# Optimization experiments

Measured on AMD Instinct MI355X. Metric: run time of the kernel, lower is better.

## Reference

```python
import jax, jax.numpy as jnp
import numpy as np

B, S, D, H = 2, 2048, 1024, 16
HD = D // H  # head_dim = 64


def setup_inputs() -> dict:
    key = jax.random.key(0)
    ks = jax.random.split(key, 10)
    std = 1.0 / np.sqrt(D)
    inputs = jax.random.normal(ks[0], (B, S, D), dtype=jnp.float32)
    # stacked per-head projection weights: [H, HD, D] (row-major like nn.Linear)
    Wq = jax.random.uniform(ks[1], (H, HD, D), jnp.float32, -std, std)
    bq = jax.random.uniform(ks[2], (H, HD), jnp.float32, -std, std)
    Wk = jax.random.uniform(ks[3], (H, HD, D), jnp.float32, -std, std)
    bk = jax.random.uniform(ks[4], (H, HD), jnp.float32, -std, std)
    Wv = jax.random.uniform(ks[5], (H, HD, D), jnp.float32, -std, std)
    bv = jax.random.uniform(ks[6], (H, HD), jnp.float32, -std, std)
    Wo = jax.random.uniform(ks[7], (D, D), jnp.float32, -std, std)
    bo = jax.random.uniform(ks[8], (D,), jnp.float32, -std, std)
    return {"inputs": inputs, "Wq": Wq, "bq": bq, "Wk": Wk, "bk": bk,
            "Wv": Wv, "bv": bv, "Wo": Wo, "bo": bo}


def reference(inputs, Wq, bq, Wk, bk, Wv, bv, Wo, bo):
    # per-head projections, batched over heads: [B,H,S,HD]
    q = jnp.einsum('bsd,hed->bhse', inputs, Wq) + bq[None, :, None, :]
    k = jnp.einsum('bsd,hed->bhse', inputs, Wk) + bk[None, :, None, :]
    v = jnp.einsum('bsd,hed->bhse', inputs, Wv) + bv[None, :, None, :]
    scale = 1.0 / np.sqrt(HD).astype(np.float32)
    # explicit [B,H,S,S] score matrix, as in the original naive attention
    scores = jnp.einsum('bhqe,bhke->bhqk', q, k) * scale
    causal = jnp.tril(jnp.ones((S, S), dtype=bool))
    scores = jnp.where(causal[None, None], scores, jnp.float32(-jnp.inf))
    attn = jax.nn.softmax(scores, axis=-1)  # dropout p=0 -> identity
    wv = jnp.einsum('bhqk,bhke->bhqe', attn, v)
    # concat heads along feature dim: [B,S,H*HD] = [B,S,D]
    z = wv.transpose(0, 2, 1, 3).reshape(B, S, D)
    out = jnp.einsum('bsd,ed->bse', z, Wo) + bo
    return out
```

## Files before the change

kernel.cpp:

```cpp
#include <hip/hip_runtime.h>
#include <math.h>

#define Bx 2
#define Sx 2048
#define Dx 1024
#define Hx 16
#define HDx 64
#define Mx (Bx*Sx)

typedef __bf16 bf16x8 __attribute__((ext_vector_type(8)));
typedef __bf16 bf16x4 __attribute__((ext_vector_type(4)));
typedef float  f32x4  __attribute__((ext_vector_type(4)));

#define SCL 0.18033688011112042f

__device__ __forceinline__ void gload_lds16(const __bf16* g, __bf16* l) {
  __builtin_amdgcn_global_load_lds(
      (const __attribute__((address_space(1))) unsigned int*)g,
      (__attribute__((address_space(3))) unsigned int*)l, 16, 0, 0);
}

__device__ __forceinline__ void cvt8(const float* s, __bf16* d) {
  float4 a = *(const float4*)s;
  float4 b = *(const float4*)(s + 4);
  bf16x8 o;
  o[0] = (__bf16)a.x; o[1] = (__bf16)a.y; o[2] = (__bf16)a.z; o[3] = (__bf16)a.w;
  o[4] = (__bf16)b.x; o[5] = (__bf16)b.y; o[6] = (__bf16)b.z; o[7] = (__bf16)b.w;
  *(bf16x8*)d = o;
}

__global__ __launch_bounds__(256) void cvt_kernel(
    const float* __restrict__ x, const float* __restrict__ Wq,
    const float* __restrict__ Wk, const float* __restrict__ Wv,
    const float* __restrict__ Wo, const float* __restrict__ bq,
    const float* __restrict__ bk, const float* __restrict__ bv,
    __bf16* __restrict__ xb, __bf16* __restrict__ wqkv,
    __bf16* __restrict__ wob, float* __restrict__ bqkv)
{
  const int bid = blockIdx.x;
  const int t = threadIdx.x;
  const size_t MEG = 1024u * 1024u;
  if (bid < 2048) {
    size_t e = (size_t)bid * 2048 + t * 8;
    cvt8(x + e, xb + e);
  } else if (bid < 3584) {
    size_t e = (size_t)(bid - 2048) * 2048 + t * 8;
    const float* src = (e < MEG) ? (Wq + e) : (e < 2 * MEG) ? (Wk + (e - MEG)) : (Wv + (e - 2 * MEG));
    cvt8(src, wqkv + e);
  } else if (bid < 4096) {
    size_t e = (size_t)(bid - 3584) * 2048 + t * 8;
    cvt8(Wo + e, wob + e);
  } else {
    for (int i = t; i < 3072; i += 256)
      bqkv[i] = (i < 1024) ? bq[i] : (i < 2048) ? bk[i - 1024] : bv[i - 2048];
  }
}

template<int TM, int TN, int MODE>
__global__ __launch_bounds__(256) void gemm_k(
    const __bf16* __restrict__ A, const __bf16* __restrict__ W,
    const float* __restrict__ bias, float* __restrict__ Cf,
    __bf16* __restrict__ Cb, __bf16* __restrict__ vT,
    int M, int N, int K, int ldc)
{
  __shared__ __align__(16) char smem[2 * (TM + TN) * 64 * 2];
  __bf16* AsB = (__bf16*)smem;

  constexpr int MS = TM / 32;
  constexpr int NS = TN / 32;
  const int tid = threadIdx.x;
  const int lane = tid & 63, wave = tid >> 6;
  const int l16 = lane & 15, quad = lane >> 4;
  const int wm = (wave >> 1) * (TM / 2);
  const int wn = (wave & 1) * (TN / 2);
  const int swz = l16 & 7;

  const int lid = blockIdx.y * gridDim.x + blockIdx.x;
  const int g8 = lid >> 6;
  const int r64 = lid & 63;
  const int gpm = (int)gridDim.y >> 3;
  const int gm = g8 % gpm;
  const int gn = g8 / gpm;
  const int m0 = (gm * 8 + (r64 & 7)) * TM;
  const int n0 = (gn * 8 + (r64 >> 3)) * TN;

  const f32x4 zero = {0.f, 0.f, 0.f, 0.f};
  f32x4 acc[MS][NS];
#pragma unroll
  for (int i = 0; i < MS; ++i)
#pragma unroll
    for (int j = 0; j < NS; ++j) acc[i][j] = zero;

  const int srow = tid >> 3;
  const int scs = (tid & 7) ^ (srow & 7);
  const __bf16* Ag = A + (size_t)(m0 + srow) * K + scs * 8;
  const __bf16* Wg = W + (size_t)(n0 + srow) * K + scs * 8;

#define G_STAGE(k0_, b_)                                                        \
  { __bf16* As_ = AsB + (b_) * (TM + TN) * 64;                                  \
    __bf16* Bs_ = As_ + TM * 64;                                                \
    _Pragma("unroll")                                                           \
    for (int i = 0; i < TM / 32; ++i)                                           \
      gload_lds16(Ag + (size_t)(i * 32) * K + (k0_), &As_[(i * 256 + tid) * 8]);\
    _Pragma("unroll")                                                           \
    for (int i = 0; i < TN / 32; ++i)                                           \
      gload_lds16(Wg + (size_t)(i * 32) * K + (k0_), &Bs_[(i * 256 + tid) * 8]); }

  const int NT = K >> 6;
  G_STAGE(0, 0)
  __syncthreads();

  for (int t = 0; t < NT; ++t) {
    if (t + 1 < NT) G_STAGE((t + 1) << 6, (t + 1) & 1)
    const __bf16* As_ = AsB + (t & 1) * (TM + TN) * 64;
    const __bf16* Bs_ = As_ + TM * 64;
#pragma unroll
    for (int hk = 0; hk < 2; ++hk) {
      const int ph = ((hk * 4 + quad) ^ swz) * 8;
      bf16x8 af[MS], bfr[NS];
#pragma unroll
      for (int i = 0; i < MS; ++i)
        af[i] = *(const bf16x8*)&As_[(wm + i * 16 + l16) * 64 + ph];
#pragma unroll
      for (int j = 0; j < NS; ++j)
        bfr[j] = *(const bf16x8*)&Bs_[(wn + j * 16 + l16) * 64 + ph];
#pragma unroll
      for (int i = 0; i < MS; ++i)
#pragma unroll
        for (int j = 0; j < NS; ++j)
          acc[i][j] = __builtin_amdgcn_mfma_f32_16x16x32_bf16(af[i], bfr[j], acc[i][j], 0, 0, 0);
    }
    __syncthreads();
  }

  if (MODE == 0) {
    float* Cs = (float*)smem;
    constexpr int cst = TN + 4;
#pragma unroll
    for (int j = 0; j < NS; ++j) {
      const int c = wn + j * 16 + l16;
      const float bv_ = bias[n0 + c];
#pragma unroll
      for (int i = 0; i < MS; ++i) {
        const int r0 = wm + i * 16 + quad * 4;
#pragma unroll
        for (int g = 0; g < 4; ++g)
          Cs[(r0 + g) * cst + c] = acc[i][j][g] + bv_;
      }
    }
    __syncthreads();
    constexpr int passes = TM * TN / (256 * 4);
#pragma unroll
    for (int p = 0; p < passes; ++p) {
      const int slot = p * 256 + tid;
      const int row = slot / (TN / 4);
      const int col4 = (slot % (TN / 4)) * 4;
      f32x4 v = *(const f32x4*)&Cs[row * cst + col4];
      *(f32x4*)&Cf[(size_t)(m0 + row) * ldc + n0 + col4] = v;
    }
  } else {
    __bf16* Cs = (__bf16*)smem;
    constexpr int cst = TN + 8;
    const bool vtile = (n0 >= 2048);
    if (!vtile) {
#pragma unroll
      for (int j = 0; j < NS; ++j) {
        const int c = wn + j * 16 + l16;
        const float bv_ = bias[n0 + c];
        const float sc = ((n0 + c) < 1024) ? SCL : 1.0f;
#pragma unroll
        for (int i = 0; i < MS; ++i) {
          const int r0 = wm + i * 16 + quad * 4;
#pragma unroll
          for (int g = 0; g < 4; ++g)
            Cs[(r0 + g) * cst + c] = (__bf16)((acc[i][j][g] + bv_) * sc);
        }
      }
      __syncthreads();
      constexpr int passes = TM * TN / (256 * 8);
#pragma unroll
      for (int p = 0; p < passes; ++p) {
        const int slot = p * 256 + tid;
        const int row = slot / (TN / 8);
        const int col8 = (slot % (TN / 8)) * 8;
        bf16x8 v = *(const bf16x8*)&Cs[row * cst + col8];
        *(bf16x8*)&Cb[(size_t)(m0 + row) * 3072 + n0 + col8] = v;
      }
    } else {
      constexpr int cstT = TM + 8;
#pragma unroll
      for (int j = 0; j < NS; ++j) {
        const int c = wn + j * 16 + l16;
        const float bv_ = bias[n0 + c];
#pragma unroll
        for (int i = 0; i < MS; ++i) {
          const int r0 = wm + i * 16 + quad * 4;
#pragma unroll
          for (int g = 0; g < 4; ++g)
            Cs[c * cstT + r0 + g] = (__bf16)(acc[i][j][g] + bv_);
        }
      }
      __syncthreads();
      const int bb = m0 >> 11, ml = m0 & 2047;
      constexpr int passes = TM * TN / (256 * 8);
#pragma unroll
      for (int p = 0; p < passes; ++p) {
        const int slot = p * 256 + tid;
        const int dd = slot / (TM / 8);
        const int ss8 = (slot % (TM / 8)) * 8;
        bf16x8 v = *(const bf16x8*)&Cs[dd * cstT + ss8];
        const int c2 = n0 - 2048 + dd;
        const int hh = c2 >> 6, ddd = c2 & 63;
        *(bf16x8*)&vT[((size_t)(bb * 16 + hh) * 64 + ddd) * 2048 + ml + ss8] = v;
      }
    }
  }
}

__global__ __launch_bounds__(256) void attn_mfma(
    const __bf16* __restrict__ qkv, const __bf16* __restrict__ vT,
    __bf16* __restrict__ zb)
{
  __shared__ __bf16 Qs[64 * 64];
  __shared__ __bf16 Ks[2][64 * 64];
  __shared__ __bf16 Vs[3][64 * 64];

  const int tid = threadIdx.x;
  const int lane = tid & 63, wave = tid >> 6;
  const int l16 = lane & 15, quad = lane >> 4;
  const int bx = blockIdx.x;
  const int qt = 31 - (bx >> 5);
  const int bh = bx & 31;
  const int h = bh & 15, b = bh >> 4;
  const int q0 = qt * 64;

  const __bf16* qg = qkv + (size_t)b * 2048 * 3072 + h * 64;
  const __bf16* kg = qg + 1024;
  const __bf16* vg = vT + (size_t)bh * 64 * 2048;

#define STAGE_KV(kt_, kbuf, vbuf)                                               \
  { const int kn = (kt_) * 64;                                                  \
    _Pragma("unroll")                                                           \
    for (int i = 0; i < 2; ++i) {                                               \
      int slot = i * 256 + tid;                                                 \
      int row = slot >> 3, ph2 = slot & 7;                                      \
      int cs = ph2 ^ (row & 7);                                                 \
      gload_lds16(kg + (size_t)(kn + row) * 3072 + cs * 8, &Ks[kbuf][slot * 8]);\
      gload_lds16(vg + (size_t)row * 2048 + kn + cs * 8, &Vs[vbuf][slot * 8]);  \
    } }

#pragma unroll
  for (int i = 0; i < 2; ++i) {
    int slot = i * 256 + tid;
    int row = slot >> 3, ph2 = slot & 7;
    int cs = ph2 ^ (row & 7);
    gload_lds16(qg + (size_t)(q0 + row) * 3072 + cs * 8, &Qs[slot * 8]);
  }
  STAGE_KV(0, 0, 0)
  __syncthreads();

  const int swz = l16 & 7;
  const int sw0 = ((quad) ^ swz) * 8;
  const int sw1 = ((quad + 4) ^ swz) * 8;
  const int mrow = wave * 16 + l16;

  bf16x8 qf0 = *(const bf16x8*)&Qs[mrow * 64 + sw0];
  bf16x8 qf1 = *(const bf16x8*)&Qs[mrow * 64 + sw1];
  __bf16* P = &Qs[wave * 16 * 64];

  bf16x8 onesf;
  {
    __bf16 ov = (l16 == 0) ? (__bf16)1.0f : (__bf16)0.0f;
#pragma unroll
    for (int i = 0; i < 8; ++i) onesf[i] = ov;
  }

  const f32x4 zero = {0.f, 0.f, 0.f, 0.f};
  f32x4 O[4], Ol = zero;
#pragma unroll
  for (int j = 0; j < 4; ++j) O[j] = zero;
  f32x4 s_cur[4], s_next[4];

#define S_TILE(sdst, kb)                                                        \
  { _Pragma("unroll")                                                           \
    for (int m = 0; m < 4; ++m) sdst[m] = zero;                                 \
    _Pragma("unroll")                                                           \
    for (int m = 0; m < 4; ++m) {                                               \
      bf16x8 kf0 = *(const bf16x8*)&Ks[kb][(m * 16 + l16) * 64 + sw0];          \
      sdst[m] = __builtin_amdgcn_mfma_f32_16x16x32_bf16(kf0, qf0, sdst[m],0,0,0);\
      bf16x8 kf1 = *(const bf16x8*)&Ks[kb][(m * 16 + l16) * 64 + sw1];          \
      sdst[m] = __builtin_amdgcn_mfma_f32_16x16x32_bf16(kf1, qf1, sdst[m],0,0,0);\
    } }

#define EXP_P(s, DIAG)                                                          \
  { _Pragma("unroll")                                                           \
    for (int m = 0; m < 4; ++m) {                                               \
      const int kl = m * 16 + quad * 4;                                         \
      bf16x4 st;                                                                \
      _Pragma("unroll")                                                         \
      for (int g = 0; g < 4; ++g) {                                             \
        float p = __builtin_exp2f(s[m][g]);                                     \
        if (DIAG && (kl + g) > (wave * 16 + l16)) p = 0.f;                      \
        st[g] = (__bf16)p;                                                      \
      }                                                                         \
      *(bf16x4*)&P[l16 * 64 + (((2 * m + (quad >> 1)) ^ swz) * 8) + (quad & 1) * 4] = st; \
    } }

#define PV_TILE(vb)                                                             \
  { bf16x8 pf0 = *(const bf16x8*)&P[l16 * 64 + sw0];                            \
    bf16x8 pf1 = *(const bf16x8*)&P[l16 * 64 + sw1];                            \
    _Pragma("unroll")                                                           \
    for (int j = 0; j < 4; ++j) {                                               \
      bf16x8 vf0 = *(const bf16x8*)&Vs[vb][(j * 16 + l16) * 64 + sw0];          \
      O[j] = __builtin_amdgcn_mfma_f32_16x16x32_bf16(pf0, vf0, O[j], 0, 0, 0);  \
      bf16x8 vf1 = *(const bf16x8*)&Vs[vb][(j * 16 + l16) * 64 + sw1];          \
      O[j] = __builtin_amdgcn_mfma_f32_16x16x32_bf16(pf1, vf1, O[j], 0, 0, 0);  \
    }                                                                           \
    Ol = __builtin_amdgcn_mfma_f32_16x16x32_bf16(pf0, onesf, Ol, 0, 0, 0);      \
    Ol = __builtin_amdgcn_mfma_f32_16x16x32_bf16(pf1, onesf, Ol, 0, 0, 0); }

  if (qt > 0) STAGE_KV(1, 1, 1)
  S_TILE(s_cur, 0)
  if (qt > 0) __syncthreads();

  for (int t = 0; t < qt; ++t) {
    EXP_P(s_cur, false)
    S_TILE(s_next, (t + 1) & 1)
    PV_TILE(t % 3)
    if (t + 2 <= qt) STAGE_KV(t + 2, t & 1, (t + 2) % 3)
    __syncthreads();
#pragma unroll
    for (int m = 0; m < 4; ++m) s_cur[m] = s_next[m];
  }
  EXP_P(s_cur, true)
  PV_TILE(qt % 3)

  const int rq = q0 + wave * 16 + quad * 4;
#pragma unroll
  for (int g = 0; g < 4; ++g) {
    const float lv = __shfl(Ol[g], quad * 16);
    const float inv = 1.0f / lv;
    const size_t rb = (size_t)(b * 2048 + rq + g) * 1024 + h * 64 + l16;
#pragma unroll
    for (int j = 0; j < 4; ++j)
      zb[rb + j * 16] = (__bf16)(O[j][g] * inv);
  }
}

extern "C" void kernel_launch(void* const* d_in, const int* in_sizes, int n_in,
                              void* d_out, int out_size, void* d_ws, size_t ws_size,
                              hipStream_t stream) {
  (void)in_sizes; (void)n_in; (void)out_size; (void)ws_size;
  const float* x  = (const float*)d_in[0];
  const float* Wq = (const float*)d_in[1];
  const float* bq = (const float*)d_in[2];
  const float* Wk = (const float*)d_in[3];
  const float* bk = (const float*)d_in[4];
  const float* Wv = (const float*)d_in[5];
  const float* bv = (const float*)d_in[6];
  const float* Wo = (const float*)d_in[7];
  const float* bo = (const float*)d_in[8];

  char* ws = (char*)d_ws;
  __bf16* xb   = (__bf16*)(ws);
  __bf16* wqkv = (__bf16*)(ws + (8ull  << 20));
  __bf16* wob  = (__bf16*)(ws + (14ull << 20));
  float*  bqkv = (float*) (ws + (16ull << 20));
  __bf16* qkv  = (__bf16*)(ws + (17ull << 20));
  __bf16* vT   = (__bf16*)(ws + (41ull << 20));
  __bf16* zb   = (__bf16*)(ws + (49ull << 20));

  cvt_kernel<<<4097, 256, 0, stream>>>(x, Wq, Wk, Wv, Wo, bq, bk, bv,
                                       xb, wqkv, wob, bqkv);
  gemm_k<128, 128, 1><<<dim3(24, 32), 256, 0, stream>>>(
      xb, wqkv, bqkv, nullptr, qkv, vT, Mx, 3072, 1024, 0);
  attn_mfma<<<1024, 256, 0, stream>>>(qkv, vT, zb);
  gemm_k<128, 64, 0><<<dim3(16, 32), 256, 0, stream>>>(
      zb, wob, bo, (float*)d_out, nullptr, nullptr, Mx, 1024, 1024, 1024);
}
```

Baseline: 177.2 us.

## Widen attention query tile to 128 rows per block to reuse K/V tiles

After: 188.1 us. 1.06x slower.

```diff
diff --git a/kernel.cpp b/kernel.cpp
--- a/kernel.cpp
+++ b/kernel.cpp
@@ -217,11 +217,11 @@
   }
 }
 
-__global__ __launch_bounds__(256) void attn_mfma(
+__global__ __launch_bounds__(256, 2) void attn_mfma(
     const __bf16* __restrict__ qkv, const __bf16* __restrict__ vT,
     __bf16* __restrict__ zb)
 {
-  __shared__ __bf16 Qs[64 * 64];
+  __shared__ __bf16 Qs[128 * 64];
   __shared__ __bf16 Ks[2][64 * 64];
   __shared__ __bf16 Vs[3][64 * 64];
 
@@ -229,10 +229,12 @@
   const int lane = tid & 63, wave = tid >> 6;
   const int l16 = lane & 15, quad = lane >> 4;
   const int bx = blockIdx.x;
-  const int qt = 31 - (bx >> 5);
-  const int bh = bx & 31;
+  const int jj = bx & 255;
+  const int bh = jj & 31;
+  const int gg = jj >> 5;
+  const int qt = (bx >> 8) ? gg : (15 - gg);
+  const int q0 = qt * 128;
   const int h = bh & 15, b = bh >> 4;
-  const int q0 = qt * 64;
 
   const __bf16* qg = qkv + (size_t)b * 2048 * 3072 + h * 64;
   const __bf16* kg = qg + 1024;
@@ -250,7 +252,7 @@
     } }
 
 #pragma unroll
-  for (int i = 0; i < 2; ++i) {
+  for (int i = 0; i < 4; ++i) {
     int slot = i * 256 + tid;
     int row = slot >> 3, ph2 = slot & 7;
     int cs = ph2 ^ (row & 7);
@@ -260,13 +262,17 @@
   __syncthreads();
 
   const int swz = l16 & 7;
-  const int sw0 = ((quad) ^ swz) * 8;
+  const int sw0 = (quad ^ swz) * 8;
   const int sw1 = ((quad + 4) ^ swz) * 8;
-  const int mrow = wave * 16 + l16;
-
-  bf16x8 qf0 = *(const bf16x8*)&Qs[mrow * 64 + sw0];
-  bf16x8 qf1 = *(const bf16x8*)&Qs[mrow * 64 + sw1];
-  __bf16* P = &Qs[wave * 16 * 64];
+
+  bf16x8 qf0[2], qf1[2];
+#pragma unroll
+  for (int n = 0; n < 2; ++n) {
+    const int r = wave * 32 + n * 16 + l16;
+    qf0[n] = *(const bf16x8*)&Qs[r * 64 + sw0];
+    qf1[n] = *(const bf16x8*)&Qs[r * 64 + sw1];
+  }
+  __bf16* P = &Qs[wave * 32 * 64];
 
   bf16x8 onesf;
   {
@@ -276,74 +282,97 @@
   }
 
   const f32x4 zero = {0.f, 0.f, 0.f, 0.f};
-  f32x4 O[4], Ol = zero;
-#pragma unroll
-  for (int j = 0; j < 4; ++j) O[j] = zero;
-  f32x4 s_cur[4], s_next[4];
+  f32x4 O[4][2], Ol[2];
+#pragma unroll
+  for (int j = 0; j < 4; ++j) { O[j][0] = zero; O[j][1] = zero; }
+  Ol[0] = zero; Ol[1] = zero;
+  f32x4 s_cur[4][2], s_next[4][2];
 
 #define S_TILE(sdst, kb)                                                        \
   { _Pragma("unroll")                                                           \
-    for (int m = 0; m < 4; ++m) sdst[m] = zero;                                 \
-    _Pragma("unroll")                                                           \
     for (int m = 0; m < 4; ++m) {                                               \
       bf16x8 kf0 = *(const bf16x8*)&Ks[kb][(m * 16 + l16) * 64 + sw0];          \
-      sdst[m] = __builtin_amdgcn_mfma_f32_16x16x32_bf16(kf0, qf0, sdst[m],0,0,0);\
       bf16x8 kf1 = *(const bf16x8*)&Ks[kb][(m * 16 + l16) * 64 + sw1];          \
-      sdst[m] = __builtin_amdgcn_mfma_f32_16x16x32_bf16(kf1, qf1, sdst[m],0,0,0);\
-    } }
-
-#define EXP_P(s, DIAG)                                                          \
+      _Pragma("unroll")                                                         \
+      for (int n = 0; n < 2; ++n) {                                             \
+        sdst[m][n] = zero;                                                      \
+        sdst[m][n] = __builtin_amdgcn_mfma_f32_16x16x32_bf16(kf0, qf0[n], sdst[m][n],0,0,0); \
+        sdst[m][n] = __builtin_amdgcn_mfma_f32_16x16x32_bf16(kf1, qf1[n], sdst[m][n],0,0,0); \
+      } } }
+
+#define EXP_P(s, DIAG, KOFF)                                                    \
   { _Pragma("unroll")                                                           \
     for (int m = 0; m < 4; ++m) {                                               \
-      const int kl = m * 16 + quad * 4;                                         \
-      bf16x4 st;                                                                \
+      const int kl = (KOFF) + m * 16 + quad * 4;                                \
       _Pragma("unroll")                                                         \
-      for (int g = 0; g < 4; ++g) {                                             \
-        float p = __builtin_exp2f(s[m][g]);                                     \
-        if (DIAG && (kl + g) > (wave * 16 + l16)) p = 0.f;                      \
-        st[g] = (__bf16)p;                                                      \
-      }                                                                         \
-      *(bf16x4*)&P[l16 * 64 + (((2 * m + (quad >> 1)) ^ swz) * 8) + (quad & 1) * 4] = st; \
-    } }
+      for (int n = 0; n < 2; ++n) {                                             \
+        const int ql = wave * 32 + n * 16 + l16;                                \
+        bf16x4 st;                                                              \
+        _Pragma("unroll")                                                       \
+        for (int g = 0; g < 4; ++g) {                                           \
+          float p = __builtin_exp2f(s[m][n][g]);                                \
+          if (DIAG && (kl + g) > ql) p = 0.f;                                   \
+          st[g] = (__bf16)p;                                                    \
+        }                                                                       \
+        *(bf16x4*)&P[n * 1024 + l16 * 64 + (((2 * m + (quad >> 1)) ^ swz) * 8) + (quad & 1) * 4] = st; \
+      } } }
 
 #define PV_TILE(vb)                                                             \
-  { bf16x8 pf0 = *(const bf16x8*)&P[l16 * 64 + sw0];                            \
-    bf16x8 pf1 = *(const bf16x8*)&P[l16 * 64 + sw1];                            \
+  { bf16x8 pf0[2], pf1[2];                                                      \
+    _Pragma("unroll")                                                           \
+    for (int n = 0; n < 2; ++n) {                                               \
+      pf0[n] = *(const bf16x8*)&P[n * 1024 + l16 * 64 + sw0];                   \
+      pf1[n] = *(const bf16x8*)&P[n * 1024 + l16 * 64 + sw1];                   \
+    }                                                                           \
     _Pragma("unroll")                                                           \
     for (int j = 0; j < 4; ++j) {                                               \
       bf16x8 vf0 = *(const bf16x8*)&Vs[vb][(j * 16 + l16) * 64 + sw0];          \
-      O[j] = __builtin_amdgcn_mfma_f32_16x16x32_bf16(pf0, vf0, O[j], 0, 0, 0);  \
       bf16x8 vf1 = *(const bf16x8*)&Vs[vb][(j * 16 + l16) * 64 + sw1];          \
-      O[j] = __builtin_amdgcn_mfma_f32_16x16x32_bf16(pf1, vf1, O[j], 0, 0, 0);  \
+      _Pragma("unroll")                                                         \
+      for (int n = 0; n < 2; ++n) {                                             \
+        O[j][n] = __builtin_amdgcn_mfma_f32_16x16x32_bf16(pf0[n], vf0, O[j][n], 0, 0, 0); \
+        O[j][n] = __builtin_amdgcn_mfma_f32_16x16x32_bf16(pf1[n], vf1, O[j][n], 0, 0, 0); \
+      }                                                                         \
     }                                                                           \
-    Ol = __builtin_amdgcn_mfma_f32_16x16x32_bf16(pf0, onesf, Ol, 0, 0, 0);      \
-    Ol = __builtin_amdgcn_mfma_f32_16x16x32_bf16(pf1, onesf, Ol, 0, 0, 0); }
-
-  if (qt > 0) STAGE_KV(1, 1, 1)
+    _Pragma("unroll")                                                           \
+    for (int n = 0; n < 2; ++n) {                                               \
+      Ol[n] = __builtin_amdgcn_mfma_f32_16x16x32_bf16(pf0[n], onesf, Ol[n], 0, 0, 0); \
+      Ol[n] = __builtin_amdgcn_mfma_f32_16x16x32_bf16(pf1[n], onesf, Ol[n], 0, 0, 0); \
+    } }
+
+  const int NT = 2 * qt + 2;
+
+  STAGE_KV(1, 1, 1)
   S_TILE(s_cur, 0)
-  if (qt > 0) __syncthreads();
-
-  for (int t = 0; t < qt; ++t) {
-    EXP_P(s_cur, false)
-    S_TILE(s_next, (t + 1) & 1)
+  __syncthreads();
+
+  for (int t = 0; t < NT - 1; ++t) {
+    if (t < NT - 2) { EXP_P(s_cur, false, 0) }
+    else            { EXP_P(s_cur, true, 0) }
+    if (t < NT - 2 || wave >= 2) S_TILE(s_next, (t + 1) & 1)
     PV_TILE(t % 3)
-    if (t + 2 <= qt) STAGE_KV(t + 2, t & 1, (t + 2) % 3)
+    if (t + 2 < NT) STAGE_KV(t + 2, t & 1, (t + 2) % 3)
     __syncthreads();
 #pragma unroll
-    for (int m = 0; m < 4; ++m) s_cur[m] = s_next[m];
-  }
-  EXP_P(s_cur, true)
-  PV_TILE(qt % 3)
-
-  const int rq = q0 + wave * 16 + quad * 4;
-#pragma unroll
-  for (int g = 0; g < 4; ++g) {
-    const float lv = __shfl(Ol[g], quad * 16);
-    const float inv = 1.0f / lv;
-    const size_t rb = (size_t)(b * 2048 + rq + g) * 1024 + h * 64 + l16;
-#pragma unroll
-    for (int j = 0; j < 4; ++j)
-      zb[rb + j * 16] = (__bf16)(O[j][g] * inv);
+    for (int m = 0; m < 4; ++m) { s_cur[m][0] = s_next[m][0]; s_cur[m][1] = s_next[m][1]; }
+  }
+  if (wave >= 2) {
+    EXP_P(s_cur, true, 64)
+    PV_TILE((NT - 1) % 3)
+  }
+
+#pragma unroll
+  for (int n = 0; n < 2; ++n) {
+    const int rq = q0 + wave * 32 + n * 16 + quad * 4;
+#pragma unroll
+    for (int g = 0; g < 4; ++g) {
+      const float lv = __shfl(Ol[n][g], quad * 16);
+      const float inv = 1.0f / lv;
+      const size_t rb = (size_t)(b * 2048 + rq + g) * 1024 + h * 64 + l16;
+#pragma unroll
+      for (int j = 0; j < 4; ++j)
+        zb[rb + j * 16] = (__bf16)(O[j][n][g] * inv);
+    }
   }
 }
 
@@ -374,7 +403,7 @@
                                        xb, wqkv, wob, bqkv);
   gemm_k<128, 128, 1><<<dim3(24, 32), 256, 0, stream>>>(
       xb, wqkv, bqkv, nullptr, qkv, vT, Mx, 3072, 1024, 0);
-  attn_mfma<<<1024, 256, 0, stream>>>(qkv, vT, zb);
+  attn_mfma<<<512, 256, 0, stream>>>(qkv, vT, zb);
   gemm_k<128, 64, 0><<<dim3(16, 32), 256, 0, stream>>>(
       zb, wob, bo, (float*)d_out, nullptr, nullptr, Mx, 1024, 1024, 1024);
 }
```

## Rebalance attention tile order, double-buffer V, and raise MFMA priority

Applied to the files above, without the earlier changes.

Result: slower. 183.2 us (+3.4%).

```diff
diff --git a/kernel.cpp b/kernel.cpp
--- a/kernel.cpp
+++ b/kernel.cpp
@@ -217,20 +217,22 @@
   }
 }
 
-__global__ __launch_bounds__(256) void attn_mfma(
+__global__ __launch_bounds__(256, 4) void attn_mfma(
     const __bf16* __restrict__ qkv, const __bf16* __restrict__ vT,
     __bf16* __restrict__ zb)
 {
   __shared__ __bf16 Qs[64 * 64];
   __shared__ __bf16 Ks[2][64 * 64];
-  __shared__ __bf16 Vs[3][64 * 64];
+  __shared__ __bf16 Vs[2][64 * 64];
 
   const int tid = threadIdx.x;
   const int lane = tid & 63, wave = tid >> 6;
   const int l16 = lane & 15, quad = lane >> 4;
   const int bx = blockIdx.x;
-  const int qt = 31 - (bx >> 5);
   const int bh = bx & 31;
+  const int s8 = (bx >> 5) & 7;
+  const int p4 = bx >> 8;
+  const int qt = (p4 == 0) ? s8 : (p4 == 1) ? 15 - s8 : (p4 == 2) ? 16 + s8 : 31 - s8;
   const int h = bh & 15, b = bh >> 4;
   const int q0 = qt * 64;
 
@@ -238,7 +240,7 @@
   const __bf16* kg = qg + 1024;
   const __bf16* vg = vT + (size_t)bh * 64 * 2048;
 
-#define STAGE_KV(kt_, kbuf, vbuf)                                               \
+#define STAGE_K(kt_, kbuf)                                                      \
   { const int kn = (kt_) * 64;                                                  \
     _Pragma("unroll")                                                           \
     for (int i = 0; i < 2; ++i) {                                               \
@@ -246,6 +248,15 @@
       int row = slot >> 3, ph2 = slot & 7;                                      \
       int cs = ph2 ^ (row & 7);                                                 \
       gload_lds16(kg + (size_t)(kn + row) * 3072 + cs * 8, &Ks[kbuf][slot * 8]);\
+    } }
+
+#define STAGE_V(kt_, vbuf)                                                      \
+  { const int kn = (kt_) * 64;                                                  \
+    _Pragma("unroll")                                                           \
+    for (int i = 0; i < 2; ++i) {                                               \
+      int slot = i * 256 + tid;                                                 \
+      int row = slot >> 3, ph2 = slot & 7;                                      \
+      int cs = ph2 ^ (row & 7);                                                 \
       gload_lds16(vg + (size_t)row * 2048 + kn + cs * 8, &Vs[vbuf][slot * 8]);  \
     } }
 
@@ -256,7 +267,8 @@
     int cs = ph2 ^ (row & 7);
     gload_lds16(qg + (size_t)(q0 + row) * 3072 + cs * 8, &Qs[slot * 8]);
   }
-  STAGE_KV(0, 0, 0)
+  STAGE_K(0, 0)
+  STAGE_V(0, 0)
   __syncthreads();
 
   const int swz = l16 & 7;
@@ -282,7 +294,8 @@
   f32x4 s_cur[4], s_next[4];
 
 #define S_TILE(sdst, kb)                                                        \
-  { _Pragma("unroll")                                                           \
+  { __builtin_amdgcn_s_setprio(1);                                              \
+    _Pragma("unroll")                                                           \
     for (int m = 0; m < 4; ++m) sdst[m] = zero;                                 \
     _Pragma("unroll")                                                           \
     for (int m = 0; m < 4; ++m) {                                               \
@@ -290,7 +303,8 @@
       sdst[m] = __builtin_amdgcn_mfma_f32_16x16x32_bf16(kf0, qf0, sdst[m],0,0,0);\
       bf16x8 kf1 = *(const bf16x8*)&Ks[kb][(m * 16 + l16) * 64 + sw1];          \
       sdst[m] = __builtin_amdgcn_mfma_f32_16x16x32_bf16(kf1, qf1, sdst[m],0,0,0);\
-    } }
+    }                                                                           \
+    __builtin_amdgcn_s_setprio(0); }
 
 #define EXP_P(s, DIAG)                                                          \
   { _Pragma("unroll")                                                           \
@@ -309,6 +323,7 @@
 #define PV_TILE(vb)                                                             \
   { bf16x8 pf0 = *(const bf16x8*)&P[l16 * 64 + sw0];                            \
     bf16x8 pf1 = *(const bf16x8*)&P[l16 * 64 + sw1];                            \
+    __builtin_amdgcn_s_setprio(1);                                              \
     _Pragma("unroll")                                                           \
     for (int j = 0; j < 4; ++j) {                                               \
       bf16x8 vf0 = *(const bf16x8*)&Vs[vb][(j * 16 + l16) * 64 + sw0];          \
@@ -317,23 +332,25 @@
       O[j] = __builtin_amdgcn_mfma_f32_16x16x32_bf16(pf1, vf1, O[j], 0, 0, 0);  \
     }                                                                           \
     Ol = __builtin_amdgcn_mfma_f32_16x16x32_bf16(pf0, onesf, Ol, 0, 0, 0);      \
-    Ol = __builtin_amdgcn_mfma_f32_16x16x32_bf16(pf1, onesf, Ol, 0, 0, 0); }
-
-  if (qt > 0) STAGE_KV(1, 1, 1)
+    Ol = __builtin_amdgcn_mfma_f32_16x16x32_bf16(pf1, onesf, Ol, 0, 0, 0);      \
+    __builtin_amdgcn_s_setprio(0); }
+
+  STAGE_K(1, 1)
   S_TILE(s_cur, 0)
-  if (qt > 0) __syncthreads();
+  __syncthreads();
 
   for (int t = 0; t < qt; ++t) {
     EXP_P(s_cur, false)
+    STAGE_V(t + 1, (t + 1) & 1)
+    if (t + 2 <= qt) STAGE_K(t + 2, t & 1)
     S_TILE(s_next, (t + 1) & 1)
-    PV_TILE(t % 3)
-    if (t + 2 <= qt) STAGE_KV(t + 2, t & 1, (t + 2) % 3)
+    PV_TILE(t & 1)
     __syncthreads();
 #pragma unroll
     for (int m = 0; m < 4; ++m) s_cur[m] = s_next[m];
   }
   EXP_P(s_cur, true)
-  PV_TILE(qt % 3)
+  PV_TILE(qt & 1)
 
   const int rq = q0 + wave * 16 + quad * 4;
 #pragma unroll
```

## Replace QKV projection GEMM with 256x256-tile 8-wave pipelined kernel

Applied to the files above, without the earlier changes.

Result: no change. 178.7 us (+0.8%).

```diff
diff --git a/kernel.cpp b/kernel.cpp
--- a/kernel.cpp
+++ b/kernel.cpp
@@ -217,6 +217,190 @@
   }
 }
 
+__global__ __launch_bounds__(512, 1) void gemm8_qkv(
+    const __bf16* __restrict__ A, const __bf16* __restrict__ W,
+    const float* __restrict__ bias, __bf16* __restrict__ Cb,
+    __bf16* __restrict__ vT)
+{
+  __shared__ __align__(16) char smem8[131072];
+
+  const int tid = threadIdx.x;
+  const int lane = tid & 63;
+  const int wid = tid >> 6;
+  const int l16 = lane & 15, quad = lane >> 4;
+  const int wm = (wid >> 2) * 128;
+  const int wn = (wid & 3) * 64;
+  const int swz = l16 & 7;
+
+  const int lid = blockIdx.x;
+  const int wg = (lid & 7) * 24 + (lid >> 3);
+  const int m0 = (wg / 12) * 256;
+  const int n0 = (wg % 12) * 256;
+
+  const int r0 = tid >> 3;
+  const int r1 = r0 + 64;
+  const int ch8 = tid & 7;
+  const int cs0 = ch8 ^ (r0 & 7);
+  const int cs1 = ch8 ^ (r1 & 7);
+
+  const __bf16* Ag0 = A + (size_t)(m0 + r0) * 1024 + cs0 * 8;
+  const __bf16* Ag1 = A + (size_t)(m0 + r1) * 1024 + cs1 * 8;
+  const __bf16* Wg0 = W + (size_t)(n0 + r0) * 1024 + cs0 * 8;
+  const __bf16* Wg1 = W + (size_t)(n0 + r1) * 1024 + cs1 * 8;
+
+#define LA8(b) ((__bf16*)(smem8 + (b) * 65536))
+#define LB8(b) ((__bf16*)(smem8 + (b) * 65536 + 32768))
+
+#define STG_A(half, kt) {                                                      \
+    __bf16* d_ = LA8((kt) & 1) + (half) * 8192;                                \
+    const size_t o_ = (size_t)(half) * 131072 + (size_t)(kt) * 64;             \
+    gload_lds16(Ag0 + o_, d_ + tid * 8);                                       \
+    gload_lds16(Ag1 + o_, d_ + (512 + tid) * 8); }
+#define STG_B(half, kt) {                                                      \
+    __bf16* d_ = LB8((kt) & 1) + (half) * 8192;                                \
+    const size_t o_ = (size_t)(half) * 131072 + (size_t)(kt) * 64;             \
+    gload_lds16(Wg0 + o_, d_ + tid * 8);                                       \
+    gload_lds16(Wg1 + o_, d_ + (512 + tid) * 8); }
+
+#define RDA(f, kh, mh, b) (*(const bf16x8*)&LA8(b)[(wm + ((mh)*4+(f))*16 + l16) * 64 + ((((kh)*4+quad)) ^ swz) * 8])
+#define RDB(n, kh, nh, b) (*(const bf16x8*)&LB8(b)[(wn + ((nh)*2+(n))*16 + l16) * 64 + ((((kh)*4+quad)) ^ swz) * 8])
+
+  const f32x4 zero = {0.f, 0.f, 0.f, 0.f};
+  f32x4 acc[8][4];
+#pragma unroll
+  for (int i = 0; i < 8; ++i)
+#pragma unroll
+    for (int j = 0; j < 4; ++j) acc[i][j] = zero;
+
+#define MQ(a_, b_, mh, nh) {                                                   \
+    _Pragma("unroll")                                                          \
+    for (int f_ = 0; f_ < 4; ++f_)                                             \
+      _Pragma("unroll")                                                        \
+      for (int n_ = 0; n_ < 2; ++n_) {                                         \
+        acc[(mh)*4+f_][(nh)*2+n_] = __builtin_amdgcn_mfma_f32_16x16x32_bf16(   \
+            a_[f_][0], b_[n_][0], acc[(mh)*4+f_][(nh)*2+n_], 0, 0, 0);         \
+        acc[(mh)*4+f_][(nh)*2+n_] = __builtin_amdgcn_mfma_f32_16x16x32_bf16(   \
+            a_[f_][1], b_[n_][1], acc[(mh)*4+f_][(nh)*2+n_], 0, 0, 0); } }
+
+#define KTB(kt, cur) {                                                         \
+    const bool st_ = (kt) < 14;                                                \
+    bf16x8 af[4][2], bfl[2][2], bfh[2][2];                                     \
+            \
+    _Pragma("unroll")                                                          \
+    for (int f_ = 0; f_ < 4; ++f_) { af[f_][0] = RDA(f_,0,0,cur); af[f_][1] = RDA(f_,1,0,cur); } \
+    _Pragma("unroll")                                                          \
+    for (int n_ = 0; n_ < 2; ++n_) { bfl[n_][0] = RDB(n_,0,0,cur); bfl[n_][1] = RDB(n_,1,0,cur); } \
+    __builtin_amdgcn_s_barrier();                                              \
+    __builtin_amdgcn_s_setprio(1);                                             \
+    MQ(af, bfl, 0, 0)                                                          \
+    __builtin_amdgcn_s_setprio(0);                                             \
+    __builtin_amdgcn_s_barrier();                                              \
+                                       \
+    _Pragma("unroll")                                                          \
+    for (int n_ = 0; n_ < 2; ++n_) { bfh[n_][0] = RDB(n_,0,1,cur); bfh[n_][1] = RDB(n_,1,1,cur); } \
+    __builtin_amdgcn_s_barrier();                                              \
+    __builtin_amdgcn_s_setprio(1);                                             \
+    MQ(af, bfh, 0, 1)                                                          \
+    __builtin_amdgcn_s_setprio(0);                                             \
+    __builtin_amdgcn_s_barrier();                                              \
+           \
+    _Pragma("unroll")                                                          \
+    for (int f_ = 0; f_ < 4; ++f_) { af[f_][0] = RDA(f_,0,1,cur); af[f_][1] = RDA(f_,1,1,cur); } \
+    if (st_) { STG_B(0, (kt) + 2) STG_B(1, (kt) + 2) }                         \
+    __builtin_amdgcn_s_barrier();                                              \
+    __builtin_amdgcn_s_setprio(1);                                             \
+    MQ(af, bfl, 1, 0)                                                          \
+    __builtin_amdgcn_s_setprio(0);                                             \
+    __builtin_amdgcn_s_barrier();                                              \
+              \
+    if (st_) { STG_A(0, (kt) + 2) STG_A(1, (kt) + 2)                           \
+               asm volatile("s_waitcnt vmcnt(8)" ::: "memory"); }              \
+    else     { asm volatile("s_waitcnt vmcnt(0)" ::: "memory"); }              \
+    __builtin_amdgcn_s_barrier();                                              \
+    __builtin_amdgcn_s_setprio(1);                                             \
+    MQ(af, bfh, 1, 1)                                                          \
+    __builtin_amdgcn_s_setprio(0);                                             \
+    __builtin_amdgcn_s_barrier(); }
+
+  STG_A(0, 0) STG_B(0, 0) STG_B(1, 0) STG_A(1, 0)
+  STG_A(0, 1) STG_B(0, 1) STG_B(1, 1) STG_A(1, 1)
+  asm volatile("s_waitcnt vmcnt(0)" ::: "memory");
+  __builtin_amdgcn_s_barrier();
+
+  for (int i2 = 0; i2 < 8; ++i2) {
+    KTB(2 * i2, 0)
+    KTB(2 * i2 + 1, 1)
+  }
+  __syncthreads();
+
+  const bool vtile = (n0 >= 2048);
+  if (!vtile) {
+    const float sc = (n0 < 1024) ? SCL : 1.0f;
+    __bf16* Cs = (__bf16*)smem8;
+#pragma unroll
+    for (int h = 0; h < 2; ++h) {
+      if ((wid >> 2) == h) {
+#pragma unroll
+        for (int f = 0; f < 8; ++f) {
+          const int rl = f * 16 + quad * 4;
+#pragma unroll
+          for (int nf = 0; nf < 4; ++nf) {
+            const int c = wn + nf * 16 + l16;
+            const float bv_ = bias[n0 + c];
+#pragma unroll
+            for (int g = 0; g < 4; ++g)
+              Cs[(rl + g) * 264 + c] = (__bf16)((acc[f][nf][g] + bv_) * sc);
+          }
+        }
+      }
+      __syncthreads();
+#pragma unroll
+      for (int p = 0; p < 8; ++p) {
+        const int slot = p * 512 + tid;
+        const int row = slot >> 5;
+        const int c8 = (slot & 31) * 8;
+        bf16x8 v = *(const bf16x8*)&Cs[row * 264 + c8];
+        *(bf16x8*)&Cb[(size_t)(m0 + h * 128 + row) * 3072 + n0 + c8] = v;
+      }
+      __syncthreads();
+    }
+  } else {
+    __bf16* Cs = (__bf16*)smem8;
+    const int bb = m0 >> 11, ml = m0 & 2047;
+#pragma unroll
+    for (int chf = 0; chf < 2; ++chf) {
+      if (((wid & 3) >> 1) == chf) {
+#pragma unroll
+        for (int f = 0; f < 8; ++f) {
+          const int r = wm + f * 16 + quad * 4;
+#pragma unroll
+          for (int nf = 0; nf < 4; ++nf) {
+            const int cl = (wn + nf * 16 + l16) - chf * 128;
+            const float bv_ = bias[n0 + chf * 128 + cl];
+            bf16x4 ov = (bf16x4){(__bf16)(acc[f][nf][0] + bv_),
+                                 (__bf16)(acc[f][nf][1] + bv_),
+                                 (__bf16)(acc[f][nf][2] + bv_),
+                                 (__bf16)(acc[f][nf][3] + bv_)};
+            *(bf16x4*)&Cs[cl * 264 + r] = ov;
+          }
+        }
+      }
+      __syncthreads();
+#pragma unroll
+      for (int p = 0; p < 8; ++p) {
+        const int slot = p * 512 + tid;
+        const int dd = slot >> 5;
+        const int s8 = (slot & 31) * 8;
+        bf16x8 v = *(const bf16x8*)&Cs[dd * 264 + s8];
+        const int c2 = n0 - 2048 + chf * 128 + dd;
+        const int hh = c2 >> 6, ddd = c2 & 63;
+        *(bf16x8*)&vT[((size_t)(bb * 16 + hh) * 64 + ddd) * 2048 + ml + s8] = v;
+      }
+      __syncthreads();
+    }
+  }
+}
+
 __global__ __launch_bounds__(256) void attn_mfma(
     const __bf16* __restrict__ qkv, const __bf16* __restrict__ vT,
     __bf16* __restrict__ zb)
@@ -372,8 +556,7 @@
 
   cvt_kernel<<<4097, 256, 0, stream>>>(x, Wq, Wk, Wv, Wo, bq, bk, bv,
                                        xb, wqkv, wob, bqkv);
-  gemm_k<128, 128, 1><<<dim3(24, 32), 256, 0, stream>>>(
-      xb, wqkv, bqkv, nullptr, qkv, vT, Mx, 3072, 1024, 0);
+  gemm8_qkv<<<192, 512, 0, stream>>>(xb, wqkv, bqkv, qkv, vT);
   attn_mfma<<<1024, 256, 0, stream>>>(qkv, vT, zb);
   gemm_k<128, 64, 0><<<dim3(16, 32), 256, 0, stream>>>(
       zb, wob, bo, (float*)d_out, nullptr, nullptr, Mx, 1024, 1024, 1024);
```
